# Optimization experiments

Hardware: AMD Instinct MI355X
Metric: run time of the kernel (lower is better)

Reference implementation:

```python
import jax, jax.numpy as jnp
import numpy as np

DIM = 128
NUM_SLOTS = 8
ITERS = 3
EPS = 1e-8
LN_EPS = 1e-3
HIDDEN = max(DIM, 128)


def _ln(x, w, b):
    mu = jnp.mean(x, axis=-1, keepdims=True)
    var = jnp.mean(jnp.square(x - mu), axis=-1, keepdims=True)
    return (x - mu) * jax.lax.rsqrt(var + LN_EPS) * w + b


def setup_inputs() -> dict:
    key = jax.random.key(0)
    ks = jax.random.split(key, 16)
    b, n, d, h = 32, 4096, DIM, HIDDEN
    limit = np.sqrt(6.0 / (1 + d))
    inp = {
        'inputs': jax.random.normal(ks[0], (b, n, d), jnp.float32),
        'slots_mu': jax.random.uniform(ks[1], (1, 1, d), jnp.float32, -limit, limit),
        'slots_log_sigma': jax.random.uniform(ks[2], (1, 1, d), jnp.float32, -limit, limit),
        'Wq': jax.random.normal(ks[3], (d, d), jnp.float32) / np.sqrt(d),
        'Wk': jax.random.normal(ks[4], (d, d), jnp.float32) / np.sqrt(d),
        'Wv': jax.random.normal(ks[5], (d, d), jnp.float32) / np.sqrt(d),
        'W_ih': jax.random.normal(ks[6], (3 * d, d), jnp.float32) / np.sqrt(d),
        'W_hh': jax.random.normal(ks[7], (3 * d, d), jnp.float32) / np.sqrt(d),
        'b_ih': jnp.zeros((3 * d,), jnp.float32),
        'b_hh': jnp.zeros((3 * d,), jnp.float32),
        'W1': jax.random.normal(ks[8], (h, d), jnp.float32) / np.sqrt(d),
        'b1': jnp.zeros((h,), jnp.float32),
        'W2': jax.random.normal(ks[9], (d, h), jnp.float32) / np.sqrt(h),
        'b2': jnp.zeros((d,), jnp.float32),
        'ln_in_w': jnp.ones((d,), jnp.float32), 'ln_in_b': jnp.zeros((d,), jnp.float32),
        'ln_s_w': jnp.ones((d,), jnp.float32), 'ln_s_b': jnp.zeros((d,), jnp.float32),
        'ln_ff_w': jnp.ones((d,), jnp.float32), 'ln_ff_b': jnp.zeros((d,), jnp.float32),
    }
    return inp


def reference(inputs, slots_mu, slots_log_sigma, Wq, Wk, Wv, W_ih, W_hh, b_ih, b_hh,
              W1, b1, W2, b2, ln_in_w, ln_in_b, ln_s_w, ln_s_b, ln_ff_w, ln_ff_b):
    b, n, d = inputs.shape
    scale = d ** -0.5
    # stochastic slot init (reparameterized, fixed key for determinism)
    noise = jax.random.normal(jax.random.key(42), (b, NUM_SLOTS, d), inputs.dtype)
    slots = slots_mu + jnp.exp(slots_log_sigma) * noise

    x = _ln(inputs, ln_in_w, ln_in_b)
    k = jnp.einsum('bnd,ed->bne', x, Wk)
    v = jnp.einsum('bnd,ed->bne', x, Wv)

    for _ in range(ITERS):
        slots_prev = slots
        q = jnp.einsum('bsd,ed->bse', _ln(slots, ln_s_w, ln_s_b), Wq)
        dots = jnp.einsum('bid,bjd->bij', q, k) * scale          # [b, slots, n]
        attn = jax.nn.softmax(dots, axis=1) + EPS                 # softmax over slots
        attn = attn / jnp.sum(attn, axis=-1, keepdims=True)       # normalize over tokens
        updates = jnp.einsum('bjd,bij->bid', v, attn)             # [b, slots, d]
        # GRUCell(updates, slots_prev)
        gx = jnp.einsum('bsd,ed->bse', updates, W_ih) + b_ih
        gh = jnp.einsum('bsd,ed->bse', slots_prev, W_hh) + b_hh
        xr, xz, xn = jnp.split(gx, 3, axis=-1)
        hr, hz, hn = jnp.split(gh, 3, axis=-1)
        r = jax.nn.sigmoid(xr + hr)
        z = jax.nn.sigmoid(xz + hz)
        ng = jnp.tanh(xn + r * hn)
        slots = (1.0 - z) * ng + z * slots_prev
        # residual MLP
        ff = _ln(slots, ln_ff_w, ln_ff_b)
        ff = jax.nn.relu(jnp.einsum('bsd,hd->bsh', ff, W1) + b1)
        slots = slots + jnp.einsum('bsh,dh->bsd', ff, W2) + b2
    return slots
```

## Files before the change

### kernel.cpp

```cpp
#include <hip/hip_runtime.h>
#include <hip/hip_bf16.h>
#include <math.h>

#define DIM 128
#define NSLOT 8
#define NTOK 4096
#define NB 32
#define CHUNK 128
#define NCH (NTOK / CHUNK)
#define CHUNKPAD 136
#define LN_EPS 1e-3f
#define ATT_EPS 1e-8f
#define SCALE 0.08838834764831845f

#define BM 64
#define LDK 136

typedef short bf16x8 __attribute__((ext_vector_type(8)));
typedef float f32x4 __attribute__((ext_vector_type(4)));
typedef unsigned short ushort8_t __attribute__((ext_vector_type(8)));

__device__ __forceinline__ float bf2f(unsigned short u) {
  return __uint_as_float(((unsigned)u) << 16);
}
__device__ __forceinline__ unsigned short f2bf(float f) {
  unsigned u = __float_as_uint(f);
  unsigned r = (u + 0x7FFFu + ((u >> 16) & 1u)) >> 16;
  return (unsigned short)r;
}

__device__ __forceinline__ float erfinv_like_xla(float x) {
  double xd = (double)x;
  double w = -log1p(-xd * xd);
  double p;
  if (w < 5.0) {
    w = w - 2.5;
    p = 2.81022636e-08;
    p = 3.43273939e-07 + p * w;
    p = -3.5233877e-06 + p * w;
    p = -4.39150654e-06 + p * w;
    p = 0.00021858087 + p * w;
    p = -0.00125372503 + p * w;
    p = -0.00417768164 + p * w;
    p = 0.246640727 + p * w;
    p = 1.50140941 + p * w;
  } else {
    w = sqrt(w) - 3.0;
    p = -0.000200214257;
    p = 0.000100950558 + p * w;
    p = 0.00134934322 + p * w;
    p = -0.00367342844 + p * w;
    p = 0.00573950773 + p * w;
    p = -0.0076224613 + p * w;
    p = 0.00943887047 + p * w;
    p = 1.00167406 + p * w;
    p = 2.83297682 + p * w;
  }
  return (float)(p * xd);
}

__global__ __launch_bounds__(256) void k_init_slots(
    const float* __restrict__ mu, const float* __restrict__ lsig,
    float* __restrict__ slots, const float* __restrict__ Wk,
    const float* __restrict__ Wv, unsigned short* __restrict__ Wbf,
    const float* __restrict__ Wq, const float* __restrict__ lnw,
    const float* __restrict__ lnb, unsigned short* __restrict__ qbf) {
  int b = blockIdx.x, t = threadIdx.x;
  __shared__ __align__(16) float sc[NSLOT][DIM];
  __shared__ __align__(16) float sln[NSLOT][DIM];

#pragma unroll
  for (int u = 0; u < 2; ++u) {
    int i = b * 512 + u * 256 + t;
    Wbf[i] = f2bf(Wk[i]);
    Wbf[DIM * DIM + i] = f2bf(Wv[i]);
  }

#pragma unroll
  for (int r4 = 0; r4 < 4; ++r4) {
    int idx = b * 1024 + r4 * 256 + t;
    uint32_t x0 = 0u, x1 = (uint32_t)idx;
    uint32_t k0 = 0u, k1 = 42u;
    uint32_t ks[3] = {k0, k1, k0 ^ k1 ^ 0x1BD11BDAu};
    x0 += ks[0];
    x1 += ks[1];
    const int rot[2][4] = {{13, 15, 26, 6}, {17, 29, 16, 24}};
#pragma unroll
    for (int blk = 0; blk < 5; ++blk) {
      const int* r = rot[blk & 1];
#pragma unroll
      for (int j = 0; j < 4; ++j) {
        x0 += x1;
        x1 = (x1 << r[j]) | (x1 >> (32 - r[j]));
        x1 ^= x0;
      }
      x0 += ks[(blk + 1) % 3];
      x1 += ks[(blk + 2) % 3] + (uint32_t)(blk + 1);
    }
    uint32_t bits = x0 ^ x1;
    float f = __uint_as_float((bits >> 9) | 0x3F800000u) - 1.0f;
    const float mn = __uint_as_float(0xBF7FFFFFu);
    float u = fmaxf(f * 2.0f + mn, mn);
    float noise = 1.41421356f * erfinv_like_xla(u);
    int d = idx & (DIM - 1);
    float val = mu[d] + expf(lsig[d]) * noise;
    slots[idx] = val;
    int li = r4 * 256 + t;
    sc[li >> 7][li & (DIM - 1)] = val;
  }
  __syncthreads();

  {
    int s = t >> 5, c = t & 31;
    float4 xv = *reinterpret_cast<const float4*>(&sc[s][c * 4]);
    float ps = xv.x + xv.y + xv.z + xv.w;
    float pq = xv.x * xv.x + xv.y * xv.y + xv.z * xv.z + xv.w * xv.w;
#pragma unroll
    for (int m = 16; m >= 1; m >>= 1) {
      ps += __shfl_xor(ps, m, 32);
      pq += __shfl_xor(pq, m, 32);
    }
    float mean = ps * (1.0f / DIM);
    float var = fmaxf(pq * (1.0f / DIM) - mean * mean, 0.0f);
    float inv = 1.0f / sqrtf(var + LN_EPS);
    float vals[4] = {xv.x, xv.y, xv.z, xv.w};
#pragma unroll
    for (int ii = 0; ii < 4; ++ii) {
      int d = c * 4 + ii;
      sln[s][d] = (vals[ii] - mean) * inv * lnw[d] + lnb[d];
    }
  }
  __syncthreads();
  {
    int s = t >> 5, c = t & 31;
#pragma unroll
    for (int ii = 0; ii < 4; ++ii) {
      int e = c + 32 * ii;
      const float* wr = Wq + e * DIM;
      float acc = 0.0f;
#pragma unroll
      for (int d4 = 0; d4 < DIM / 4; ++d4) {
        float4 w4 = *reinterpret_cast<const float4*>(wr + d4 * 4);
        float4 s4 = *reinterpret_cast<const float4*>(&sln[s][d4 * 4]);
        acc += s4.x * w4.x + s4.y * w4.y + s4.z * w4.z + s4.w * w4.w;
      }
      qbf[(b * NSLOT + s) * DIM + e] = f2bf(SCALE * acc);
    }
  }
}

__global__ __launch_bounds__(512) void k_ln_kv(
    const float* __restrict__ inp, const unsigned short* __restrict__ Wbf,
    const float* __restrict__ lnw, const float* __restrict__ lnb,
    unsigned short* __restrict__ kt, unsigned short* __restrict__ vt) {
  __shared__ __align__(16) unsigned short A[BM * LDK];
  __shared__ __align__(16) unsigned short Bv[DIM * 72];
  int t = threadIdx.x;
  int tg = blockIdx.x;

  {
    int r = t >> 3, p = t & 7;
    const float* src = inp + ((size_t)tg * BM + r) * DIM + p * 16;
    float xr[16];
    float s = 0.f, sq = 0.f;
#pragma unroll
    for (int i4 = 0; i4 < 4; ++i4) {
      float4 v = *reinterpret_cast<const float4*>(src + i4 * 4);
      xr[i4 * 4 + 0] = v.x; xr[i4 * 4 + 1] = v.y;
      xr[i4 * 4 + 2] = v.z; xr[i4 * 4 + 3] = v.w;
      s += v.x + v.y + v.z + v.w;
      sq += v.x * v.x + v.y * v.y + v.z * v.z + v.w * v.w;
    }
    s += __shfl_xor(s, 1); sq += __shfl_xor(sq, 1);
    s += __shfl_xor(s, 2); sq += __shfl_xor(sq, 2);
    s += __shfl_xor(s, 4); sq += __shfl_xor(sq, 4);
    float mean = s * (1.0f / DIM);
    float var = fmaxf(sq * (1.0f / DIM) - mean * mean, 0.0f);
    float inv = 1.0f / sqrtf(var + LN_EPS);
#pragma unroll
    for (int c8 = 0; c8 < 2; ++c8) {
      ushort8_t pk;
#pragma unroll
      for (int j = 0; j < 8; ++j) {
        int d = p * 16 + c8 * 8 + j;
        float y = (xr[c8 * 8 + j] - mean) * inv * lnw[d] + lnb[d];
        pk[j] = f2bf(y);
      }
      *reinterpret_cast<ushort8_t*>(&A[r * LDK + p * 16 + c8 * 8]) = pk;
    }
  }
  __syncthreads();

  int w = t >> 6, l = t & 63, lm = l & 15, lg = l >> 4;
  int mat = w >> 2;
  int ebase = (w & 3) * 32;
  const unsigned short* Wsrc = Wbf + mat * DIM * DIM;

  f32x4 acc[8];
#pragma unroll
  for (int i = 0; i < 8; ++i) acc[i] = (f32x4){0.f, 0.f, 0.f, 0.f};

  if (mat == 0) {
#pragma unroll
    for (int ks = 0; ks < 4; ++ks) {
      bf16x8 wf[2], xf[4];
#pragma unroll
      for (int et = 0; et < 2; ++et)
        wf[et] = *reinterpret_cast<const bf16x8*>(
            Wsrc + (ebase + et * 16 + lm) * DIM + ks * 32 + 8 * lg);
#pragma unroll
      for (int tt = 0; tt < 4; ++tt)
        xf[tt] = *reinterpret_cast<const bf16x8*>(
            &A[(tt * 16 + lm) * LDK + ks * 32 + 8 * lg]);
#pragma unroll
      for (int tt = 0; tt < 4; ++tt)
#pragma unroll
        for (int et = 0; et < 2; ++et)
          acc[tt * 2 + et] = __builtin_amdgcn_mfma_f32_16x16x32_bf16(
              xf[tt], wf[et], acc[tt * 2 + et], 0, 0, 0);
    }
  } else {
#pragma unroll
    for (int ks = 0; ks < 4; ++ks) {
      bf16x8 wf[2], xf[4];
#pragma unroll
      for (int et = 0; et < 2; ++et)
        wf[et] = *reinterpret_cast<const bf16x8*>(
            Wsrc + (ebase + et * 16 + lm) * DIM + ks * 32 + 8 * lg);
#pragma unroll
      for (int tt = 0; tt < 4; ++tt)
        xf[tt] = *reinterpret_cast<const bf16x8*>(
            &A[(tt * 16 + lm) * LDK + ks * 32 + 8 * lg]);
#pragma unroll
      for (int et = 0; et < 2; ++et)
#pragma unroll
        for (int tt = 0; tt < 4; ++tt)
          acc[et * 4 + tt] = __builtin_amdgcn_mfma_f32_16x16x32_bf16(
              wf[et], xf[tt], acc[et * 4 + tt], 0, 0, 0);
    }
  }
  __syncthreads();

  if (mat == 0) {
#pragma unroll
    for (int tt = 0; tt < 4; ++tt)
#pragma unroll
      for (int et = 0; et < 2; ++et)
#pragma unroll
        for (int r = 0; r < 4; ++r)
          A[(tt * 16 + 4 * lg + r) * LDK + ebase + et * 16 + lm] =
              f2bf(acc[tt * 2 + et][r]);
  } else {
#pragma unroll
    for (int et = 0; et < 2; ++et)
#pragma unroll
      for (int tt = 0; tt < 4; ++tt)
#pragma unroll
        for (int r = 0; r < 4; ++r)
          Bv[(ebase + et * 16 + 4 * lg + r) * 72 + tt * 16 + lm] =
              f2bf(acc[et * 4 + tt][r]);
  }
  __syncthreads();

  {
    size_t rowbase = (size_t)tg * BM;
#pragma unroll
    for (int u = 0; u < 2; ++u) {
      int i = u * 512 + t;
      int tok = i >> 4, off = (i & 15) * 8;
      ushort8_t vv = *reinterpret_cast<const ushort8_t*>(&A[tok * LDK + off]);
      *reinterpret_cast<ushort8_t*>(&kt[(rowbase + tok) * DIM + off]) = vv;
    }
    int bb = tg >> 6;
    int nb = (tg & 63) * BM;
#pragma unroll
    for (int u = 0; u < 2; ++u) {
      int i = u * 512 + t;
      int e = i >> 3, off = (i & 7) * 8;
      ushort8_t vv = *reinterpret_cast<const ushort8_t*>(&Bv[e * 72 + off]);
      *reinterpret_cast<ushort8_t*>(
          &vt[((size_t)bb * DIM + e) * NTOK + nb + off]) = vv;
    }
  }
}

__global__ __launch_bounds__(512, 4) void k_attn(
    const unsigned short* __restrict__ qbf, const unsigned short* __restrict__ kt,
    const unsigned short* __restrict__ vt, float* __restrict__ Np,
    float* __restrict__ Dp) {
  int bid = blockIdx.x;
  int b = bid >> 5, ch = bid & 31;
  int n0 = ch * CHUNK;
  int t = threadIdx.x;
  int wid = t >> 6, l = t & 63, lm = l & 15, lg = l >> 4;

  __shared__ __align__(16) unsigned short a_lds[NSLOT][CHUNKPAD];

  {
    const unsigned short* qb = qbf + (b * NSLOT + (lm & 7)) * DIM;
    bf16x8 aq[4];
#pragma unroll
    for (int ks = 0; ks < 4; ++ks)
      aq[ks] = *reinterpret_cast<const bf16x8*>(qb + ks * 32 + 8 * lg);
    const unsigned short* kb = kt + ((size_t)b * NTOK + n0) * DIM;
    int tok = wid * 16 + lm;
    f32x4 acc = (f32x4){0.f, 0.f, 0.f, 0.f};
#pragma unroll
    for (int ks = 0; ks < 4; ++ks) {
      bf16x8 bk = *reinterpret_cast<const bf16x8*>(
          kb + (size_t)tok * DIM + ks * 32 + 8 * lg);
      acc = __builtin_amdgcn_mfma_f32_16x16x32_bf16(aq[ks], bk, acc, 0, 0, 0);
    }
    float m4 = fmaxf(fmaxf(acc[0], acc[1]), fmaxf(acc[2], acc[3]));
    float m8 = fmaxf(m4, __shfl_xor(m4, 16));
    float e0 = expf(acc[0] - m8), e1 = expf(acc[1] - m8);
    float e2 = expf(acc[2] - m8), e3 = expf(acc[3] - m8);
    float s4 = e0 + e1 + e2 + e3;
    float s8 = s4 + __shfl_xor(s4, 16);
    float rs = 1.0f / s8;
    if (lg < 2) {
      a_lds[4 * lg + 0][tok] = f2bf(e0 * rs + ATT_EPS);
      a_lds[4 * lg + 1][tok] = f2bf(e1 * rs + ATT_EPS);
      a_lds[4 * lg + 2][tok] = f2bf(e2 * rs + ATT_EPS);
      a_lds[4 * lg + 3][tok] = f2bf(e3 * rs + ATT_EPS);
    }
  }
  __syncthreads();

  {
    float s = 0.0f;
#pragma unroll
    for (int jj = 0; jj < CHUNK / 64; ++jj) s += bf2f(a_lds[wid][l + 64 * jj]);
#pragma unroll
    for (int m = 32; m >= 1; m >>= 1) s += __shfl_xor(s, m);
    if (l == 0) Dp[(b * NCH + ch) * NSLOT + wid] = s;
  }

  {
    f32x4 acc = (f32x4){0.f, 0.f, 0.f, 0.f};
    const unsigned short* vb =
        vt + ((size_t)b * DIM + wid * 16 + lm) * NTOK + n0;
#pragma unroll
    for (int kk = 0; kk < CHUNK / 32; ++kk) {
      bf16x8 af = *reinterpret_cast<const bf16x8*>(
          &a_lds[lm & 7][kk * 32 + 8 * lg]);
      bf16x8 bv = *reinterpret_cast<const bf16x8*>(vb + kk * 32 + 8 * lg);
      acc = __builtin_amdgcn_mfma_f32_16x16x32_bf16(af, bv, acc, 0, 0, 0);
    }
    if (lg < 2) {
#pragma unroll
      for (int r = 0; r < 4; ++r)
        Np[((size_t)(b * NCH + ch) * NSLOT + 4 * lg + r) * DIM + wid * 16 +
           lm] = acc[r];
    }
  }
}

__global__ __launch_bounds__(256) void k_update(
    float* __restrict__ slots, unsigned short* __restrict__ qbf,
    const float* __restrict__ Np, const float* __restrict__ Dp,
    const float* __restrict__ W_ih, const float* __restrict__ W_hh,
    const float* __restrict__ b_ih, const float* __restrict__ b_hh,
    const float* __restrict__ W1, const float* __restrict__ b1,
    const float* __restrict__ W2, const float* __restrict__ b2,
    const float* __restrict__ lnfw, const float* __restrict__ lnfb,
    const float* __restrict__ Wq, const float* __restrict__ lnsw,
    const float* __restrict__ lnsb) {
  int bs = blockIdx.x;
  int b = bs >> 3, s = bs & 7;
  int t = threadIdx.x;
  __shared__ __align__(16) float pn[2][DIM];
  __shared__ __align__(16) float upd[DIM];
  __shared__ __align__(16) float sprev[DIM];
  __shared__ __align__(16) float snew[DIM];
  __shared__ __align__(16) float ffin[DIM];
  __shared__ __align__(16) float ffb[DIM];
  __shared__ __align__(16) float gx[3 * DIM];
  __shared__ __align__(16) float gh[3 * DIM];

  float dsum = 0.0f;
  for (int ch = 0; ch < NCH; ++ch) dsum += Dp[(b * NCH + ch) * NSLOT + s];

  {
    int d = t & (DIM - 1), h = t >> 7;
    float a = 0.0f;
    for (int ch = h * (NCH / 2); ch < (h + 1) * (NCH / 2); ++ch)
      a += Np[((size_t)(b * NCH + ch) * NSLOT + s) * DIM + d];
    pn[h][d] = a;
    if (h == 0) sprev[d] = slots[(b * NSLOT + s) * DIM + d];
  }
  __syncthreads();
  if (t < DIM) upd[t] = (pn[0][t] + pn[1][t]) / dsum;
  __syncthreads();

  for (int e = t; e < 3 * DIM; e += 256) {
    const float* wi = W_ih + e * DIM;
    const float* wh = W_hh + e * DIM;
    float ax = 0.0f, ah = 0.0f;
#pragma unroll
    for (int d4 = 0; d4 < DIM / 4; ++d4) {
      float4 u4 = *reinterpret_cast<const float4*>(&upd[d4 * 4]);
      float4 p4 = *reinterpret_cast<const float4*>(&sprev[d4 * 4]);
      float4 wi4 = *reinterpret_cast<const float4*>(wi + d4 * 4);
      float4 wh4 = *reinterpret_cast<const float4*>(wh + d4 * 4);
      ax += u4.x * wi4.x + u4.y * wi4.y + u4.z * wi4.z + u4.w * wi4.w;
      ah += p4.x * wh4.x + p4.y * wh4.y + p4.z * wh4.z + p4.w * wh4.w;
    }
    gx[e] = ax + b_ih[e];
    gh[e] = ah + b_hh[e];
  }
  __syncthreads();

  if (t < DIM) {
    float xr = gx[t], xz = gx[DIM + t], xn = gx[2 * DIM + t];
    float hr = gh[t], hz = gh[DIM + t], hn = gh[2 * DIM + t];
    float r = 1.0f / (1.0f + expf(-(xr + hr)));
    float z = 1.0f / (1.0f + expf(-(xz + hz)));
    float ng = tanhf(xn + r * hn);
    snew[t] = (1.0f - z) * ng + z * sprev[t];
  }
  __syncthreads();

  if (t < DIM) {
    float s1 = 0.0f, s2 = 0.0f;
#pragma unroll 8
    for (int d = 0; d < DIM; ++d) {
      float v = snew[d];
      s1 += v;
      s2 += v * v;
    }
    float mean = s1 * (1.0f / DIM);
    float var = fmaxf(s2 * (1.0f / DIM) - mean * mean, 0.0f);
    float inv = 1.0f / sqrtf(var + LN_EPS);
    ffin[t] = (snew[t] - mean) * inv * lnfw[t] + lnfb[t];
  }
  __syncthreads();

  if (t < DIM) {
    const float* wr = W1 + t * DIM;
    float acc = 0.0f;
#pragma unroll
    for (int d4 = 0; d4 < DIM / 4; ++d4) {
      float4 f4 = *reinterpret_cast<const float4*>(&ffin[d4 * 4]);
      float4 w4 = *reinterpret_cast<const float4*>(wr + d4 * 4);
      acc += f4.x * w4.x + f4.y * w4.y + f4.z * w4.z + f4.w * w4.w;
    }
    ffb[t] = fmaxf(acc + b1[t], 0.0f);
  }
  __syncthreads();

  if (t < DIM) {
    const float* wr = W2 + t * DIM;
    float acc = 0.0f;
#pragma unroll
    for (int h4 = 0; h4 < DIM / 4; ++h4) {
      float4 f4 = *reinterpret_cast<const float4*>(&ffb[h4 * 4]);
      float4 w4 = *reinterpret_cast<const float4*>(wr + h4 * 4);
      acc += f4.x * w4.x + f4.y * w4.y + f4.z * w4.z + f4.w * w4.w;
    }
    float val = snew[t] + acc + b2[t];
    slots[(b * NSLOT + s) * DIM + t] = val;
    gx[t] = val;
  }
  __syncthreads();

  if (t < DIM) {
    float s1 = 0.0f, s2 = 0.0f;
#pragma unroll 8
    for (int d = 0; d < DIM; ++d) {
      float v = gx[d];
      s1 += v;
      s2 += v * v;
    }
    float mean = s1 * (1.0f / DIM);
    float var = fmaxf(s2 * (1.0f / DIM) - mean * mean, 0.0f);
    float inv = 1.0f / sqrtf(var + LN_EPS);
    gh[t] = (gx[t] - mean) * inv * lnsw[t] + lnsb[t];
  }
  __syncthreads();

  if (t < DIM) {
    const float* wr = Wq + t * DIM;
    float acc = 0.0f;
#pragma unroll
    for (int d4 = 0; d4 < DIM / 4; ++d4) {
      float4 g4 = *reinterpret_cast<const float4*>(&gh[d4 * 4]);
      float4 w4 = *reinterpret_cast<const float4*>(wr + d4 * 4);
      acc += g4.x * w4.x + g4.y * w4.y + g4.z * w4.z + g4.w * w4.w;
    }
    qbf[(b * NSLOT + s) * DIM + t] = f2bf(SCALE * acc);
  }
}

__global__ __launch_bounds__(256) void k_sentinel(float* __restrict__ out,
                                                  int n) {
  int i = blockIdx.x * blockDim.x + threadIdx.x;
  if (i < n) out[i] = 1234.5f;
}

extern "C" void kernel_launch(void* const* d_in, const int* in_sizes, int n_in,
                              void* d_out, int out_size, void* d_ws,
                              size_t ws_size, hipStream_t stream) {
  const float* inp = (const float*)d_in[0];
  const float* mu = (const float*)d_in[1];
  const float* lsig = (const float*)d_in[2];
  const float* Wq = (const float*)d_in[3];
  const float* Wk = (const float*)d_in[4];
  const float* Wv = (const float*)d_in[5];
  const float* W_ih = (const float*)d_in[6];
  const float* W_hh = (const float*)d_in[7];
  const float* b_ih = (const float*)d_in[8];
  const float* b_hh = (const float*)d_in[9];
  const float* W1 = (const float*)d_in[10];
  const float* b1 = (const float*)d_in[11];
  const float* W2 = (const float*)d_in[12];
  const float* b2 = (const float*)d_in[13];
  const float* ln_in_w = (const float*)d_in[14];
  const float* ln_in_b = (const float*)d_in[15];
  const float* ln_s_w = (const float*)d_in[16];
  const float* ln_s_b = (const float*)d_in[17];
  const float* ln_ff_w = (const float*)d_in[18];
  const float* ln_ff_b = (const float*)d_in[19];

  float* slots = (float*)d_out;

  const size_t kv_elems = (size_t)NB * DIM * NTOK;
  const size_t np_elems = (size_t)NB * NCH * NSLOT * DIM;
  const size_t dp_elems = (size_t)NB * NCH * NSLOT;
  const size_t q_elems = (size_t)NB * NSLOT * DIM;
  size_t need = kv_elems * 2 * 2 + np_elems * 4 + dp_elems * 4 + q_elems * 2;
  if (ws_size < need) {
    k_sentinel<<<(out_size + 255) / 256, 256, 0, stream>>>((float*)d_out,
                                                           out_size);
    return;
  }
  char* wsb = (char*)d_ws;
  unsigned short* kt = (unsigned short*)wsb;
  unsigned short* vt = kt + kv_elems;
  float* Np = (float*)(wsb + kv_elems * 4);
  float* Dp = Np + np_elems;
  unsigned short* qbf = (unsigned short*)(Dp + dp_elems);
  unsigned short* Wbf = (unsigned short*)Np;

  k_init_slots<<<NB, 256, 0, stream>>>(mu, lsig, slots, Wk, Wv, Wbf, Wq,
                                       ln_s_w, ln_s_b, qbf);
  k_ln_kv<<<NB * NTOK / BM, 512, 0, stream>>>(inp, Wbf, ln_in_w, ln_in_b, kt,
                                              vt);
  for (int it = 0; it < 3; ++it) {
    k_attn<<<NB * NCH, 512, 0, stream>>>(qbf, kt, vt, Np, Dp);
    k_update<<<NB * NSLOT, 256, 0, stream>>>(slots, qbf, Np, Dp, W_ih, W_hh,
                                             b_ih, b_hh, W1, b1, W2, b2,
                                             ln_ff_w, ln_ff_b, Wq, ln_s_w,
                                             ln_s_b);
  }
}
```

Before: 185.8 us.

## Fuse first attention iteration into LN/KV projection kernel

The first iteration's attention (q·k dots, softmax over slots, partial numerators and denominators) is computed inside k_ln_kv while K and V tiles are still in shared memory. This removes one k_attn launch and the re-read of K/V from global memory for that iteration. Partial sums now use 64 token chunks per batch, so the workspace layout changes and the bf16 weight buffer moves to its own region. The last k_update also skips its unneeded q computation. In exchange k_ln_kv does more work per block and adds an extra barrier.

```diff
diff --git a/kernel.cpp b/kernel.cpp
--- a/kernel.cpp
+++ b/kernel.cpp
@@ -8,6 +8,7 @@
 #define NB 32
 #define CHUNK 128
 #define NCH (NTOK / CHUNK)
+#define NCH0 64
 #define CHUNKPAD 136
 #define LN_EPS 1e-3f
 #define ATT_EPS 1e-8f
@@ -152,9 +153,12 @@
 __global__ __launch_bounds__(512) void k_ln_kv(
     const float* __restrict__ inp, const unsigned short* __restrict__ Wbf,
     const float* __restrict__ lnw, const float* __restrict__ lnb,
-    unsigned short* __restrict__ kt, unsigned short* __restrict__ vt) {
+    unsigned short* __restrict__ kt, unsigned short* __restrict__ vt,
+    const unsigned short* __restrict__ qbf, float* __restrict__ Np,
+    float* __restrict__ Dp) {
   __shared__ __align__(16) unsigned short A[BM * LDK];
   __shared__ __align__(16) unsigned short Bv[DIM * 72];
+  __shared__ __align__(16) unsigned short a_lds[NSLOT][72];
   int t = threadIdx.x;
   int tg = blockIdx.x;
 
@@ -262,6 +266,8 @@
   }
   __syncthreads();
 
+  int bb = tg >> 6;
+  int g = tg & 63;
   {
     size_t rowbase = (size_t)tg * BM;
 #pragma unroll
@@ -271,8 +277,7 @@
       ushort8_t vv = *reinterpret_cast<const ushort8_t*>(&A[tok * LDK + off]);
       *reinterpret_cast<ushort8_t*>(&kt[(rowbase + tok) * DIM + off]) = vv;
     }
-    int bb = tg >> 6;
-    int nb = (tg & 63) * BM;
+    int nb = g * BM;
 #pragma unroll
     for (int u = 0; u < 2; ++u) {
       int i = u * 512 + t;
@@ -280,6 +285,61 @@
       ushort8_t vv = *reinterpret_cast<const ushort8_t*>(&Bv[e * 72 + off]);
       *reinterpret_cast<ushort8_t*>(
           &vt[((size_t)bb * DIM + e) * NTOK + nb + off]) = vv;
+    }
+  }
+
+  if (w < 4) {
+    const unsigned short* qb = qbf + (bb * NSLOT + (lm & 7)) * DIM;
+    bf16x8 aq[4];
+#pragma unroll
+    for (int ks = 0; ks < 4; ++ks)
+      aq[ks] = *reinterpret_cast<const bf16x8*>(qb + ks * 32 + 8 * lg);
+    int tok = w * 16 + lm;
+    f32x4 dac = (f32x4){0.f, 0.f, 0.f, 0.f};
+#pragma unroll
+    for (int ks = 0; ks < 4; ++ks) {
+      bf16x8 bk = *reinterpret_cast<const bf16x8*>(
+          &A[tok * LDK + ks * 32 + 8 * lg]);
+      dac = __builtin_amdgcn_mfma_f32_16x16x32_bf16(aq[ks], bk, dac, 0, 0, 0);
+    }
+    float m4 = fmaxf(fmaxf(dac[0], dac[1]), fmaxf(dac[2], dac[3]));
+    float m8 = fmaxf(m4, __shfl_xor(m4, 16));
+    float e0 = expf(dac[0] - m8), e1 = expf(dac[1] - m8);
+    float e2 = expf(dac[2] - m8), e3 = expf(dac[3] - m8);
+    float s4 = e0 + e1 + e2 + e3;
+    float s8 = s4 + __shfl_xor(s4, 16);
+    float rs = 1.0f / s8;
+    if (lg < 2) {
+      a_lds[4 * lg + 0][tok] = f2bf(e0 * rs + ATT_EPS);
+      a_lds[4 * lg + 1][tok] = f2bf(e1 * rs + ATT_EPS);
+      a_lds[4 * lg + 2][tok] = f2bf(e2 * rs + ATT_EPS);
+      a_lds[4 * lg + 3][tok] = f2bf(e3 * rs + ATT_EPS);
+    }
+  }
+  __syncthreads();
+
+  {
+    float s = bf2f(a_lds[w][l]);
+#pragma unroll
+    for (int m = 32; m >= 1; m >>= 1) s += __shfl_xor(s, m);
+    if (l == 0) Dp[(bb * NCH0 + g) * NSLOT + w] = s;
+  }
+
+  {
+    f32x4 nac = (f32x4){0.f, 0.f, 0.f, 0.f};
+#pragma unroll
+    for (int kk = 0; kk < 2; ++kk) {
+      bf16x8 af = *reinterpret_cast<const bf16x8*>(
+          &a_lds[lm & 7][kk * 32 + 8 * lg]);
+      bf16x8 bv = *reinterpret_cast<const bf16x8*>(
+          &Bv[(w * 16 + lm) * 72 + kk * 32 + 8 * lg]);
+      nac = __builtin_amdgcn_mfma_f32_16x16x32_bf16(af, bv, nac, 0, 0, 0);
+    }
+    if (lg < 2) {
+#pragma unroll
+      for (int r = 0; r < 4; ++r)
+        Np[((size_t)(bb * NCH0 + g) * NSLOT + 4 * lg + r) * DIM + w * 16 +
+           lm] = nac[r];
     }
   }
 }
@@ -365,7 +425,7 @@
     const float* __restrict__ W2, const float* __restrict__ b2,
     const float* __restrict__ lnfw, const float* __restrict__ lnfb,
     const float* __restrict__ Wq, const float* __restrict__ lnsw,
-    const float* __restrict__ lnsb) {
+    const float* __restrict__ lnsb, int nch, int do_q) {
   int bs = blockIdx.x;
   int b = bs >> 3, s = bs & 7;
   int t = threadIdx.x;
@@ -379,13 +439,13 @@
   __shared__ __align__(16) float gh[3 * DIM];
 
   float dsum = 0.0f;
-  for (int ch = 0; ch < NCH; ++ch) dsum += Dp[(b * NCH + ch) * NSLOT + s];
+  for (int ch = 0; ch < nch; ++ch) dsum += Dp[(b * nch + ch) * NSLOT + s];
 
   {
     int d = t & (DIM - 1), h = t >> 7;
     float a = 0.0f;
-    for (int ch = h * (NCH / 2); ch < (h + 1) * (NCH / 2); ++ch)
-      a += Np[((size_t)(b * NCH + ch) * NSLOT + s) * DIM + d];
+    for (int ch = h * (nch / 2); ch < (h + 1) * (nch / 2); ++ch)
+      a += Np[((size_t)(b * nch + ch) * NSLOT + s) * DIM + d];
     pn[h][d] = a;
     if (h == 0) sprev[d] = slots[(b * NSLOT + s) * DIM + d];
   }
@@ -462,6 +522,7 @@
     slots[(b * NSLOT + s) * DIM + t] = val;
     gx[t] = val;
   }
+  if (!do_q) return;
   __syncthreads();
 
   if (t < DIM) {
@@ -525,10 +586,12 @@
   float* slots = (float*)d_out;
 
   const size_t kv_elems = (size_t)NB * DIM * NTOK;
-  const size_t np_elems = (size_t)NB * NCH * NSLOT * DIM;
-  const size_t dp_elems = (size_t)NB * NCH * NSLOT;
+  const size_t np_elems = (size_t)NB * NCH0 * NSLOT * DIM;
+  const size_t dp_elems = (size_t)NB * NCH0 * NSLOT;
   const size_t q_elems = (size_t)NB * NSLOT * DIM;
-  size_t need = kv_elems * 2 * 2 + np_elems * 4 + dp_elems * 4 + q_elems * 2;
+  const size_t w_elems = (size_t)2 * DIM * DIM;
+  size_t need = kv_elems * 2 * 2 + np_elems * 4 + dp_elems * 4 + q_elems * 2 +
+                w_elems * 2;
   if (ws_size < need) {
     k_sentinel<<<(out_size + 255) / 256, 256, 0, stream>>>((float*)d_out,
                                                            out_size);
@@ -540,17 +603,24 @@
   float* Np = (float*)(wsb + kv_elems * 4);
   float* Dp = Np + np_elems;
   unsigned short* qbf = (unsigned short*)(Dp + dp_elems);
-  unsigned short* Wbf = (unsigned short*)Np;
+  unsigned short* Wbf = qbf + q_elems;
 
   k_init_slots<<<NB, 256, 0, stream>>>(mu, lsig, slots, Wk, Wv, Wbf, Wq,
                                        ln_s_w, ln_s_b, qbf);
   k_ln_kv<<<NB * NTOK / BM, 512, 0, stream>>>(inp, Wbf, ln_in_w, ln_in_b, kt,
-                                              vt);
-  for (int it = 0; it < 3; ++it) {
-    k_attn<<<NB * NCH, 512, 0, stream>>>(qbf, kt, vt, Np, Dp);
-    k_update<<<NB * NSLOT, 256, 0, stream>>>(slots, qbf, Np, Dp, W_ih, W_hh,
-                                             b_ih, b_hh, W1, b1, W2, b2,
-                                             ln_ff_w, ln_ff_b, Wq, ln_s_w,
-                                             ln_s_b);
-  }
-}
+                                              vt, qbf, Np, Dp);
+  k_update<<<NB * NSLOT, 256, 0, stream>>>(slots, qbf, Np, Dp, W_ih, W_hh,
+                                           b_ih, b_hh, W1, b1, W2, b2, ln_ff_w,
+                                           ln_ff_b, Wq, ln_s_w, ln_s_b, NCH0,
+                                           1);
+  k_attn<<<NB * NCH, 512, 0, stream>>>(qbf, kt, vt, Np, Dp);
+  k_update<<<NB * NSLOT, 256, 0, stream>>>(slots, qbf, Np, Dp, W_ih, W_hh,
+                                           b_ih, b_hh, W1, b1, W2, b2, ln_ff_w,
+                                           ln_ff_b, Wq, ln_s_w, ln_s_b, NCH,
+                                           1);
+  k_attn<<<NB * NCH, 512, 0, stream>>>(qbf, kt, vt, Np, Dp);
+  k_update<<<NB * NSLOT, 256, 0, stream>>>(slots, qbf, Np, Dp, W_ih, W_hh,
+                                           b_ih, b_hh, W1, b1, W2, b2, ln_ff_w,
+                                           ln_ff_b, Wq, ln_s_w, ln_s_b, NCH,
+                                           0);
+}
```

Measured after the change: 197.8 us. 6.5% more time.
